# Kernel tuning notes

Hardware: AMD Instinct MI355X
Metric: run time of the kernel (lower is better)

## Reference

```python
import jax, jax.numpy as jnp
import numpy as np
from jax import lax

EPS = 2e-05


def _conv2d(x, w, b, stride):
    # x: [B,C,H,W], w: [O,I,3,3] (OIHW), VALID padding
    y = lax.conv_general_dilated(x, w, (stride, stride), 'VALID',
                                 dimension_numbers=('NCHW', 'OIHW', 'NCHW'))
    return y + b[None, :, None, None]


def _reflect_pad(x):
    return jnp.pad(x, ((0, 0), (0, 0), (1, 1), (1, 1)), mode='reflect')


def _transfer(cont_feat, styl_feat):
    # cont_feat, styl_feat: [B, N, H, W]
    B, N, H, W = cont_feat.shape
    xc = cont_feat.reshape(B, N, -1)   # [B,N,Mc]
    xs = styl_feat.reshape(B, N, -1)   # [B,N,Ms]
    I = jnp.eye(N, dtype=xc.dtype)

    # whitening of content
    mc = jnp.mean(xc, axis=-1, keepdims=True)
    xc0 = xc - mc
    cov_c = jnp.einsum('bnm,bkm->bnk', xc0, xc0) / (xc0.shape[-1] - 1)
    Lc = jnp.linalg.cholesky(cov_c + EPS * I)  # eps*I regularization (torch retry loop)
    inv_Lc = jnp.linalg.inv(Lc)
    whiten = jnp.einsum('bnk,bkm->bnm', inv_Lc, xc0)

    # coloring with style statistics
    ms = jnp.mean(xs, axis=-1, keepdims=True)
    xs0 = xs - ms
    cov_s = jnp.einsum('bnm,bkm->bnk', xs0, xs0) / (xs0.shape[-1] - 1)
    Ls = jnp.linalg.cholesky(cov_s + EPS * I)
    colored = jnp.einsum('bnk,bkm->bnm', Ls, whiten) + ms
    return colored.reshape(B, N, H, W)


def setup_inputs() -> dict:
    key = jax.random.key(0)
    k1, k2, k3, k4 = jax.random.split(key, 4)
    B, C, H, W = 8, 128, 256, 256
    cont_feat = jax.random.normal(k1, (B, C, H, W), dtype=jnp.float32)
    styl_feat = jax.random.normal(k2, (B, C, H, W), dtype=jnp.float32)
    # conv params (kaiming-ish scaling)
    fan1 = C * 9
    W1 = jax.random.normal(k3, (C, C, 3, 3), dtype=jnp.float32) / np.sqrt(fan1)
    b1 = jnp.zeros((C,), dtype=jnp.float32)
    W2 = jax.random.normal(k4, (2 * C, C, 3, 3), dtype=jnp.float32) / np.sqrt(fan1)
    b2 = jnp.zeros((2 * C,), dtype=jnp.float32)
    return {'cont_feat': cont_feat, 'styl_feat': styl_feat,
            'W1': W1, 'b1': b1, 'W2': W2, 'b2': b2}


def reference(cont_feat, styl_feat, W1, b1, W2, b2):
    cs = _transfer(cont_feat, styl_feat)          # [B,C,H,W]
    x = _conv2d(_reflect_pad(cs), W1, b1, 2)      # [B,C,H/2,W/2]
    x = jax.nn.relu(x)
    out = _conv2d(_reflect_pad(x), W2, b2, 1)     # [B,2C,H/2,W/2]
    return out
```

## Files before the change

kernel.cpp:

```cpp
#include <hip/hip_runtime.h>
#include <hip/hip_bf16.h>

#define B_  8
#define C_  128
#define M_  65536
#define EPSV 2e-05f

typedef __attribute__((ext_vector_type(8))) short bf16x8;
typedef __attribute__((ext_vector_type(4))) float f32x4;

#define MFMA(a, b, c) __builtin_amdgcn_mfma_f32_16x16x32_bf16((a), (b), (c), 0, 0, 0)

__device__ __forceinline__ short f2b(float f) {
    unsigned u = __float_as_uint(f);
    u = (u + 0x7FFFu + ((u >> 16) & 1u)) >> 16;
    return (short)u;
}

__device__ __forceinline__ int swz(int px, int c) {
    return px * 256 + ((((c >> 3) ^ (px & 15)) << 4) | ((c & 7) << 1));
}

__device__ __forceinline__ int rot(int i, int k) {
    return i * 128 + ((((k >> 2) + i) & 31) << 2) + (k & 3);
}

__global__ __launch_bounds__(256) void k_prep(const float* W1, const float* W2,
                                              short* wp1, short* wp2) {
    int idx = blockIdx.x * 256 + threadIdx.x;
    if (idx < 9 * 128 * 128) {
        int c = idx & 127, o = (idx >> 7) & 127, rs = idx >> 14;
        wp1[idx] = f2b(W1[(o * 128 + c) * 9 + rs]);
    }
    idx -= 9 * 128 * 128;
    if (idx >= 0 && idx < 9 * 256 * 128) {
        int c = idx & 127, o = (idx >> 7) & 255, rs = idx >> 15;
        wp2[idx] = f2b(W2[(o * 128 + c) * 9 + rs]);
    }
}

__global__ __launch_bounds__(256, 2) void k_gram(const float* cont, const float* styl,
                                                 float* part, float* S) {
    __shared__ short ls[2][128 * 72];
    int bx = blockIdx.x;
    int chunk = bx & 31, which = (bx >> 5) & 1, b = bx >> 6;
    const float* X = (which ? styl : cont) + (size_t)b * C_ * M_ + chunk * 2048;
    int tid = threadIdx.x, lane = tid & 63, wid = tid >> 6;
    int kg = tid & 15, r0 = tid >> 4;

    float sacc[8];
    #pragma unroll
    for (int p = 0; p < 8; ++p) sacc[p] = 0.f;
    f32x4 acc[2][8];
    for (int u = 0; u < 2; ++u)
        for (int j = 0; j < 8; ++j) acc[u][j] = (f32x4){0.f, 0.f, 0.f, 0.f};

    float4 pf[8];
    #pragma unroll
    for (int p = 0; p < 8; ++p)
        pf[p] = *(const float4*)(X + (size_t)(r0 + p * 16) * M_ + kg * 4);

    for (int it = 0; it < 32; ++it) {
        short* lb = ls[it & 1];
        #pragma unroll
        for (int p = 0; p < 8; ++p) {
            int row = r0 + p * 16;
            float4 v = pf[p];
            sacc[p] += v.x + v.y + v.z + v.w;
            union { __hip_bfloat162 h[2]; unsigned long long u; } pk;
            pk.h[0] = __float22bfloat162_rn(make_float2(v.x, v.y));
            pk.h[1] = __float22bfloat162_rn(make_float2(v.z, v.w));
            *(unsigned long long*)(lb + row * 72 + kg * 4) = pk.u;
        }
        if (it < 31) {
            int kb = (it + 1) * 64;
            #pragma unroll
            for (int p = 0; p < 8; ++p)
                pf[p] = *(const float4*)(X + (size_t)(r0 + p * 16) * M_ + kb + kg * 4);
        }
        asm volatile("s_waitcnt lgkmcnt(0)" ::: "memory");
        __builtin_amdgcn_sched_barrier(0);
        __builtin_amdgcn_s_barrier();
        for (int ks = 0; ks < 2; ++ks) {
            int co = ks * 32 + (lane >> 4) * 8;
            bf16x8 a[2], bbf[8];
            for (int u = 0; u < 2; ++u) {
                int row = (wid * 2 + u) * 16 + (lane & 15);
                a[u] = *(const bf16x8*)(lb + row * 72 + co);
            }
            for (int j = 0; j < 8; ++j) {
                int row = j * 16 + (lane & 15);
                bbf[j] = *(const bf16x8*)(lb + row * 72 + co);
            }
            for (int u = 0; u < 2; ++u)
                for (int j = 0; j < 8; ++j)
                    acc[u][j] = MFMA(a[u], bbf[j], acc[u][j]);
        }
    }
    float* Sp = S + ((size_t)which * 8 + b) * 128;
    #pragma unroll
    for (int p = 0; p < 8; ++p) {
        float s = sacc[p];
        s += __shfl_xor(s, 1); s += __shfl_xor(s, 2);
        s += __shfl_xor(s, 4); s += __shfl_xor(s, 8);
        if (kg == 0) atomicAdd(&Sp[r0 + p * 16], s);
    }
    float* Pp = part + ((size_t)((which * 8 + b) * 32 + chunk)) * 16384;
    for (int u = 0; u < 2; ++u) {
        int rowb = (wid * 2 + u) * 16 + (lane >> 4) * 4;
        for (int j = 0; j < 8; ++j) {
            int col = j * 16 + (lane & 15);
            for (int e = 0; e < 4; ++e)
                Pp[(rowb + e) * 128 + col] = acc[u][j][e];
        }
    }
}

__global__ __launch_bounds__(256) void k_gsum(const float* part, float* G) {
    int idx = blockIdx.x * 256 + threadIdx.x;
    int m = idx >> 14, e = idx & 16383;
    const float* p = part + (size_t)m * 32 * 16384 + e;
    float s = 0.f;
    #pragma unroll
    for (int c = 0; c < 32; ++c) s += p[(size_t)c * 16384];
    G[idx] = s;
}

__global__ __launch_bounds__(256) void k_solve(const float* G, const float* S,
                                               short* Tb, float* Vv) {
    __shared__ float A[16384];
    __shared__ float Bm[16384];
    __shared__ float muA[128], muB[128];
    int b = blockIdx.x;
    int tid = threadIdx.x;
    int half = tid >> 7, i = tid & 127;
    const float invM = 1.f / 65536.f;
    const float invM1 = 1.f / 65535.f;
    float* M = half ? Bm : A;
    float* mu = half ? muB : muA;
    const float* Gp = G + ((size_t)(half * 8 + b)) * 16384;
    const float* Sp = S + ((size_t)(half * 8 + b)) * 128;

    mu[i] = Sp[i] * invM;
    __syncthreads();

    {
        const float4* G4 = (const float4*)Gp;
        int c4 = i & 31;
        #pragma unroll 4
        for (int bt = 0; bt < 4; ++bt) {
            float4 gv[8];
            #pragma unroll
            for (int q = 0; q < 8; ++q) gv[q] = G4[i + 128 * (bt * 8 + q)];
            #pragma unroll
            for (int q = 0; q < 8; ++q) {
                int it = bt * 8 + q;
                int r = (i >> 5) + 4 * it;
                float mur = mu[r] * 65536.f;
                float4 mc = *(const float4*)&mu[c4 * 4];
                float4 g = gv[q], cv;
                cv.x = (g.x - mur * mc.x) * invM1;
                cv.y = (g.y - mur * mc.y) * invM1;
                cv.z = (g.z - mur * mc.z) * invM1;
                cv.w = (g.w - mur * mc.w) * invM1;
                int c0 = c4 * 4;
                if (r == c0 + 0) cv.x += EPSV;
                if (r == c0 + 1) cv.y += EPSV;
                if (r == c0 + 2) cv.z += EPSV;
                if (r == c0 + 3) cv.w += EPSV;
                *(float4*)(M + r * 128 + (((c4 + r) & 31) << 2)) = cv;
            }
        }
    }
    __syncthreads();

    #pragma unroll 1
    for (int bb = 0; bb < 4; ++bb) {
        const int jb0 = bb * 32, bend = jb0 + 32;
        float t[32], u[32], t0[32];
        #pragma unroll
        for (int g = 0; g < 8; ++g) {
            float4 v = *(const float4*)(M + i * 128 + ((((jb0 >> 2) + g + i) & 31) << 2));
            t0[g * 4 + 0] = v.x; t0[g * 4 + 1] = v.y;
            t0[g * 4 + 2] = v.z; t0[g * 4 + 3] = v.w;
        }
        #pragma unroll
        for (int jj = 0; jj < 32; ++jj) {
            const int j = jb0 + jj;
            float dot = 0.f;
            #pragma unroll
            for (int kk = 0; kk < jj; ++kk)
                dot += u[kk] * M[rot(j, jb0 + kk)];
            float raw = t0[jj] - dot;
            if (i >= j) M[rot(i, j)] = raw;
            __syncthreads();
            float pr = M[rot(j, j)];
            float piv = sqrtf(pr);
            float rpj = 1.f / piv;
            float tv = (i > j) ? raw * rpj : (i == j ? piv : 0.f);
            t[jj] = tv;
            u[jj] = tv * rpj;
        }
        #pragma unroll
        for (int g = 0; g < 8; ++g) {
            float4 v = {t[g * 4], t[g * 4 + 1], t[g * 4 + 2], t[g * 4 + 3]};
            *(float4*)(M + i * 128 + ((((jb0 >> 2) + g + i) & 31) << 2)) =
                (i >= jb0) ? v : *(float4*)(M + i * 128 + ((((jb0 >> 2) + g + i) & 31) << 2));
        }
        __syncthreads();
        if (bb < 3) {
            if (i >= bend) {
                int jmax = (i & ~63) + 64;
                for (int j4 = bend; j4 < jmax; j4 += 4) {
                    float* rp_ = M + i * 128 + ((((j4 >> 2) + i) & 31) << 2);
                    float4 r = *(float4*)rp_;
                    #pragma unroll
                    for (int g = 0; g < 8; ++g) {
                        int kc = (jb0 >> 2) + g;
                        float4 c0 = *(const float4*)(M + (j4 + 0) * 128 + (((kc + j4 + 0) & 31) << 2));
                        float4 c1 = *(const float4*)(M + (j4 + 1) * 128 + (((kc + j4 + 1) & 31) << 2));
                        float4 c2 = *(const float4*)(M + (j4 + 2) * 128 + (((kc + j4 + 2) & 31) << 2));
                        float4 c3 = *(const float4*)(M + (j4 + 3) * 128 + (((kc + j4 + 3) & 31) << 2));
                        float ta = t[g * 4], tb = t[g * 4 + 1], tc = t[g * 4 + 2], td = t[g * 4 + 3];
                        r.x -= ta * c0.x + tb * c0.y + tc * c0.z + td * c0.w;
                        r.y -= ta * c1.x + tb * c1.y + tc * c1.z + td * c1.w;
                        r.z -= ta * c2.x + tb * c2.y + tc * c2.z + td * c2.w;
                        r.w -= ta * c3.x + tb * c3.y + tc * c3.z + td * c3.w;
                    }
                    *(float4*)rp_ = r;
                }
            }
            __syncthreads();
        }
    }
    __syncthreads();

    float rdia = 0.f, tii = 0.f;
    if (half == 0) {
        rdia = 1.f / A[rot(i, i)];
        tii = Bm[rot(i, i)] * rdia;
    }
    __syncthreads();
    if (half == 0) {
        A[rot(i, i)] = rdia;
        Bm[rot(i, i)] = tii;
    }
    __syncthreads();

    #pragma unroll 1
    for (int b2 = 3; b2 >= 0; --b2) {
        const int jb0 = b2 * 32, bend = jb0 + 32;
        if (half == 0) {
            float t[32], l0[32];
            #pragma unroll
            for (int g = 0; g < 8; ++g) {
                float4 v = *(const float4*)(Bm + i * 128 + ((((jb0 >> 2) + g + i) & 31) << 2));
                l0[g * 4 + 0] = v.x; l0[g * 4 + 1] = v.y;
                l0[g * 4 + 2] = v.z; l0[g * 4 + 3] = v.w;
            }
            #pragma unroll
            for (int jj = 31; jj >= 0; --jj) {
                const int j = jb0 + jj;
                float dot = (i < bend) ? tii * A[rot(i, j)] : 0.f;
                #pragma unroll
                for (int kk = jj + 1; kk < 32; ++kk) {
                    const int k = jb0 + kk;
                    dot += t[kk] * A[rot(k, j)];
                }
                float val = (l0[jj] - dot) * A[rot(j, j)];
                t[jj] = (j < i) ? val : (j == i ? tii : 0.f);
            }
            #pragma unroll
            for (int g = 0; g < 8; ++g) {
                float4 v = {t[g * 4], t[g * 4 + 1], t[g * 4 + 2], t[g * 4 + 3]};
                *(float4*)(Bm + i * 128 + ((((jb0 >> 2) + g + i) & 31) << 2)) = v;
            }
        }
        __syncthreads();
        if (jb0 > 0) {
            if (i >= jb0) {
                float th[32];
                #pragma unroll
                for (int g = 0; g < 8; ++g) {
                    float4 v = *(const float4*)(Bm + i * 128 + ((((jb0 >> 2) + g + i) & 31) << 2));
                    th[g * 4 + 0] = v.x; th[g * 4 + 1] = v.y;
                    th[g * 4 + 2] = v.z; th[g * 4 + 3] = v.w;
                }
                for (int j4 = half * 4; j4 < jb0; j4 += 8) {
                    float* rp = Bm + i * 128 + ((((j4 >> 2) + i) & 31) << 2);
                    float4 r = *(float4*)rp;
                    #pragma unroll
                    for (int kk = 0; kk < 32; ++kk) {
                        const int k = jb0 + kk;
                        float4 lc = *(const float4*)(A + k * 128 + ((((j4 >> 2) + k) & 31) << 2));
                        r.x -= th[kk] * lc.x; r.y -= th[kk] * lc.y;
                        r.z -= th[kk] * lc.z; r.w -= th[kk] * lc.w;
                    }
                    *(float4*)rp = r;
                }
            }
            __syncthreads();
        }
    }

    if (half == 0) {
        float vdot = 0.f;
        short* Tr = Tb + (size_t)b * 16384 + i * 128;
        for (int j4 = 0; j4 < 32; ++j4) {
            float4 tv = *(const float4*)(Bm + i * 128 + (((j4 + i) & 31) << 2));
            float4 mc = *(const float4*)&muA[j4 * 4];
            vdot += tv.x * mc.x + tv.y * mc.y + tv.z * mc.z + tv.w * mc.w;
            union { __hip_bfloat162 h[2]; unsigned long long u; } pk;
            pk.h[0] = __float22bfloat162_rn(make_float2(tv.x, tv.y));
            pk.h[1] = __float22bfloat162_rn(make_float2(tv.z, tv.w));
            *(unsigned long long*)(Tr + j4 * 4) = pk.u;
        }
        Vv[b * 128 + i] = muB[i] - vdot;
    }
}

__global__ __launch_bounds__(256) void k_transform(const float* cont, const short* Tb,
                                                   const float* Vv, short* colored) {
    __shared__ short ls[16384];
    char* lsb = (char*)ls;
    int bx = blockIdx.x;
    int b = bx >> 9, p0 = (bx & 511) << 7;
    int tid = threadIdx.x, lane = tid & 63, wid = tid >> 6;

    {
        int px = tid & 127, ch = tid >> 7;
        const float* Xp = cont + (size_t)b * C_ * M_ + p0 + px;
        for (int it = 0; it < 16; ++it) {
            int c0 = it * 8 + ch * 4;
            float x0 = Xp[(size_t)(c0 + 0) * M_];
            float x1 = Xp[(size_t)(c0 + 1) * M_];
            float x2 = Xp[(size_t)(c0 + 2) * M_];
            float x3 = Xp[(size_t)(c0 + 3) * M_];
            union { short s[4]; unsigned long long u; } pk;
            pk.s[0] = f2b(x0); pk.s[1] = f2b(x1); pk.s[2] = f2b(x2); pk.s[3] = f2b(x3);
            *(unsigned long long*)(lsb + swz(px, c0)) = pk.u;
        }
    }
    __syncthreads();
    f32x4 acc[8][2];
    for (int pg = 0; pg < 8; ++pg)
        for (int u = 0; u < 2; ++u) acc[pg][u] = (f32x4){0.f, 0.f, 0.f, 0.f};
    const short* Tbase = Tb + (size_t)b * 16384;
    for (int kc = 0; kc < 4; ++kc) {
        int co = kc * 32 + (lane >> 4) * 8;
        bf16x8 bfr[2], afr[8];
        for (int u = 0; u < 2; ++u) {
            int chn = (wid * 2 + u) * 16 + (lane & 15);
            bfr[u] = *(const bf16x8*)(Tbase + chn * 128 + co);
        }
        for (int pg = 0; pg < 8; ++pg) {
            int px = pg * 16 + (lane & 15);
            afr[pg] = *(const bf16x8*)(lsb + swz(px, co));
        }
        for (int pg = 0; pg < 8; ++pg)
            for (int u = 0; u < 2; ++u)
                acc[pg][u] = MFMA(afr[pg], bfr[u], acc[pg][u]);
    }
    __syncthreads();
    for (int u = 0; u < 2; ++u) {
        int chn = (wid * 2 + u) * 16 + (lane & 15);
        float vv = Vv[b * 128 + chn];
        for (int pg = 0; pg < 8; ++pg)
            for (int e = 0; e < 4; ++e) {
                int px = pg * 16 + (lane >> 4) * 4 + e;
                *(short*)(lsb + swz(px, chn)) = f2b(acc[pg][u][e] + vv);
            }
    }
    __syncthreads();
    short* dst = colored + ((size_t)b * M_ + p0) * 128;
    for (int it = 0; it < 8; ++it) {
        int gid = tid + it * 256;
        int px = gid >> 4, gr = gid & 15;
        bf16x8 v = *(const bf16x8*)(lsb + px * 256 + ((gr ^ (px & 15)) << 4));
        *(bf16x8*)(dst + (size_t)px * 128 + gr * 8) = v;
    }
}

__global__ __launch_bounds__(256) void k_conv1(const short* colored, const short* wp1,
                                               const float* b1, short* out1) {
    __shared__ short ls[130 * 128];
    char* lsb = (char*)ls;
    int x0 = blockIdx.x * 64, y = blockIdx.y, b = blockIdx.z;
    int tid = threadIdx.x, lane = tid & 63, wid = tid >> 6;

    f32x4 acc[4][2];
    for (int pg = 0; pg < 4; ++pg)
        for (int u = 0; u < 2; ++u) acc[pg][u] = (f32x4){0.f, 0.f, 0.f, 0.f};

    for (int r = 0; r < 3; ++r) {
        int grow = 2 * y - 1 + r;
        if (grow < 0) grow = -grow;
        __syncthreads();
        const short* src = colored + ((size_t)b * M_ + grow * 256) * 128;
        for (int it = 0; it < 9; ++it) {
            int gid = tid + it * 256;
            if (gid < 130 * 16) {
                int L = gid >> 4, gr = gid & 15;
                int gcol = 2 * x0 - 1 + L;
                if (gcol < 0) gcol = -gcol;
                else if (gcol > 255) gcol = 510 - gcol;
                bf16x8 v = *(const bf16x8*)(src + (size_t)gcol * 128 + gr * 8);
                *(bf16x8*)(lsb + L * 256 + ((gr ^ (L & 15)) << 4)) = v;
            }
        }
        __syncthreads();
        for (int s = 0; s < 3; ++s)
            for (int kc = 0; kc < 4; ++kc) {
                int co = kc * 32 + (lane >> 4) * 8;
                bf16x8 afr[4], bfr[2];
                for (int pg = 0; pg < 4; ++pg) {
                    int L = (pg * 16 + (lane & 15)) * 2 + s;
                    afr[pg] = *(const bf16x8*)(lsb + swz(L, co));
                }
                const short* wb = wp1 + (r * 3 + s) * 128 * 128;
                for (int u = 0; u < 2; ++u) {
                    int o = (wid * 2 + u) * 16 + (lane & 15);
                    bfr[u] = *(const bf16x8*)(wb + o * 128 + co);
                }
                for (int pg = 0; pg < 4; ++pg)
                    for (int u = 0; u < 2; ++u)
                        acc[pg][u] = MFMA(afr[pg], bfr[u], acc[pg][u]);
            }
    }
    __syncthreads();
    for (int u = 0; u < 2; ++u) {
        int o = (wid * 2 + u) * 16 + (lane & 15);
        float bias = b1[o];
        for (int pg = 0; pg < 4; ++pg)
            for (int e = 0; e < 4; ++e) {
                int px = pg * 16 + (lane >> 4) * 4 + e;
                float v = acc[pg][u][e] + bias;
                v = v > 0.f ? v : 0.f;
                *(short*)(lsb + swz(px, o)) = f2b(v);
            }
    }
    __syncthreads();
    short* dst = out1 + ((size_t)b * 16384 + y * 128 + x0) * 128;
    for (int it = 0; it < 4; ++it) {
        int gid = tid + it * 256;
        int px = gid >> 4, gr = gid & 15;
        bf16x8 v = *(const bf16x8*)(lsb + px * 256 + ((gr ^ (px & 15)) << 4));
        *(bf16x8*)(dst + (size_t)px * 128 + gr * 8) = v;
    }
}

__global__ __launch_bounds__(256) void k_conv2(const short* out1, const short* wp2,
                                               const float* b2, float* outp) {
    __shared__ short ls[66 * 128];
    char* lsb = (char*)ls;
    int x0 = blockIdx.x * 64, y = blockIdx.y, b = blockIdx.z;
    int tid = threadIdx.x, lane = tid & 63, wid = tid >> 6;

    f32x4 acc[4][4];
    for (int pg = 0; pg < 4; ++pg)
        for (int u = 0; u < 4; ++u) acc[pg][u] = (f32x4){0.f, 0.f, 0.f, 0.f};

    for (int r = 0; r < 3; ++r) {
        int grow = y - 1 + r;
        if (grow < 0) grow = -grow;
        else if (grow > 127) grow = 254 - grow;
        __syncthreads();
        const short* src = out1 + ((size_t)b * 16384 + grow * 128) * 128;
        for (int it = 0; it < 5; ++it) {
            int gid = tid + it * 256;
            if (gid < 66 * 16) {
                int L = gid >> 4, gr = gid & 15;
                int gcol = x0 - 1 + L;
                if (gcol < 0) gcol = -gcol;
                else if (gcol > 127) gcol = 254 - gcol;
                bf16x8 v = *(const bf16x8*)(src + (size_t)gcol * 128 + gr * 8);
                *(bf16x8*)(lsb + L * 256 + ((gr ^ (L & 15)) << 4)) = v;
            }
        }
        __syncthreads();
        for (int s = 0; s < 3; ++s)
            for (int kc = 0; kc < 4; ++kc) {
                int co = kc * 32 + (lane >> 4) * 8;
                bf16x8 afr[4], bfr[4];
                for (int pg = 0; pg < 4; ++pg) {
                    int L = pg * 16 + (lane & 15) + s;
                    afr[pg] = *(const bf16x8*)(lsb + swz(L, co));
                }
                const short* wb = wp2 + (r * 3 + s) * 256 * 128;
                for (int u = 0; u < 4; ++u) {
                    int o = (wid * 4 + u) * 16 + (lane & 15);
                    bfr[u] = *(const bf16x8*)(wb + o * 128 + co);
                }
                for (int pg = 0; pg < 4; ++pg)
                    for (int u = 0; u < 4; ++u)
                        acc[pg][u] = MFMA(afr[pg], bfr[u], acc[pg][u]);
            }
    }
    for (int u = 0; u < 4; ++u) {
        int o = (wid * 4 + u) * 16 + (lane & 15);
        float bias = b2[o];
        float* dst = outp + ((size_t)b * 256 + o) * 16384 + y * 128 + x0;
        for (int pg = 0; pg < 4; ++pg) {
            float4 v;
            v.x = acc[pg][u][0] + bias;
            v.y = acc[pg][u][1] + bias;
            v.z = acc[pg][u][2] + bias;
            v.w = acc[pg][u][3] + bias;
            *(float4*)(dst + pg * 16 + (lane >> 4) * 4) = v;
        }
    }
}

extern "C" void kernel_launch(void* const* d_in, const int* in_sizes, int n_in,
                              void* d_out, int out_size, void* d_ws, size_t ws_size,
                              hipStream_t stream) {
    const float* cont = (const float*)d_in[0];
    const float* styl = (const float*)d_in[1];
    const float* W1 = (const float*)d_in[2];
    const float* b1 = (const float*)d_in[3];
    const float* W2 = (const float*)d_in[4];
    const float* b2 = (const float*)d_in[5];
    float* outp = (float*)d_out;
    char* ws = (char*)d_ws;

    float* G       = (float*)(ws + 0x0);
    float* S       = (float*)(ws + 0x100000);
    short* Tb      = (short*)(ws + 0x110000);
    float* Vv      = (float*)(ws + 0x150000);
    short* wp1     = (short*)(ws + 0x160000);
    short* wp2     = (short*)(ws + 0x1A8000);
    short* colored = (short*)(ws + 0x400000);
    float* part    = (float*)(ws + 0x400000);
    short* out1    = (short*)(ws + 0x8400000);

    hipMemsetAsync(S, 0, 0x2000, stream);
    k_prep<<<1728, 256, 0, stream>>>(W1, W2, wp1, wp2);
    k_gram<<<512, 256, 0, stream>>>(cont, styl, part, S);
    k_gsum<<<1024, 256, 0, stream>>>(part, G);
    k_solve<<<8, 256, 0, stream>>>(G, S, Tb, Vv);
    k_transform<<<4096, 256, 0, stream>>>(cont, Tb, Vv, colored);
    k_conv1<<<dim3(2, 128, 8), 256, 0, stream>>>(colored, wp1, b1, out1);
    k_conv2<<<dim3(2, 128, 8), 256, 0, stream>>>(out1, wp2, b2, outp);
}
```

Before: 656.5 us.

## Stage wider 256-column tiles in gram kernel with full-wave row loads

The gram kernel now stages 256 columns per iteration in a single LDS buffer instead of 64 columns in a double buffer, so each wave loads whole 1KB row segments with all 64 lanes contiguous. Global loads are interleaved with bf16 conversion and LDS stores through two register sets, and each barrier is followed by 8 MFMA k-steps instead of 2. This is meant to coalesce global reads better and halve barrier frequency relative to compute. The cost is losing the overlap of the next tile's global prefetch with MFMA compute, plus more LDS use, which may lower occupancy, and more registers for the row sums.

```diff
diff --git a/kernel.cpp b/kernel.cpp
--- a/kernel.cpp
+++ b/kernel.cpp
@@ -41,69 +41,80 @@
 
 __global__ __launch_bounds__(256, 2) void k_gram(const float* cont, const float* styl,
                                                  float* part, float* S) {
-    __shared__ short ls[2][128 * 72];
+    __shared__ short ls[128 * 264];
     int bx = blockIdx.x;
     int chunk = bx & 31, which = (bx >> 5) & 1, b = bx >> 6;
     const float* X = (which ? styl : cont) + (size_t)b * C_ * M_ + chunk * 2048;
     int tid = threadIdx.x, lane = tid & 63, wid = tid >> 6;
-    int kg = tid & 15, r0 = tid >> 4;
-
-    float sacc[8];
+
+    float sacc[32];
     #pragma unroll
-    for (int p = 0; p < 8; ++p) sacc[p] = 0.f;
+    for (int p = 0; p < 32; ++p) sacc[p] = 0.f;
     f32x4 acc[2][8];
     for (int u = 0; u < 2; ++u)
         for (int j = 0; j < 8; ++j) acc[u][j] = (f32x4){0.f, 0.f, 0.f, 0.f};
 
-    float4 pf[8];
-    #pragma unroll
-    for (int p = 0; p < 8; ++p)
-        pf[p] = *(const float4*)(X + (size_t)(r0 + p * 16) * M_ + kg * 4);
-
-    for (int it = 0; it < 32; ++it) {
-        short* lb = ls[it & 1];
-        #pragma unroll
-        for (int p = 0; p < 8; ++p) {
-            int row = r0 + p * 16;
-            float4 v = pf[p];
-            sacc[p] += v.x + v.y + v.z + v.w;
-            union { __hip_bfloat162 h[2]; unsigned long long u; } pk;
-            pk.h[0] = __float22bfloat162_rn(make_float2(v.x, v.y));
-            pk.h[1] = __float22bfloat162_rn(make_float2(v.z, v.w));
-            *(unsigned long long*)(lb + row * 72 + kg * 4) = pk.u;
-        }
-        if (it < 31) {
-            int kb = (it + 1) * 64;
-            #pragma unroll
-            for (int p = 0; p < 8; ++p)
-                pf[p] = *(const float4*)(X + (size_t)(r0 + p * 16) * M_ + kb + kg * 4);
-        }
+    float4 pfA[8], pfB[8];
+
+#define GLOAD(pf, g)                                                              \
+    _Pragma("unroll")                                                             \
+    for (int p = 0; p < 8; ++p)                                                   \
+        pf[p] = *(const float4*)(X + (size_t)(wid + 4 * ((g) * 8 + p)) * M_ +     \
+                                 kb + lane * 4);
+
+#define GSTORE(pf, g)                                                             \
+    _Pragma("unroll")                                                             \
+    for (int p = 0; p < 8; ++p) {                                                 \
+        int row = wid + 4 * ((g) * 8 + p);                                        \
+        float4 v = pf[p];                                                         \
+        sacc[(g) * 8 + p] += v.x + v.y + v.z + v.w;                               \
+        union { __hip_bfloat162 h[2]; unsigned long long u; } pk;                 \
+        pk.h[0] = __float22bfloat162_rn(make_float2(v.x, v.y));                   \
+        pk.h[1] = __float22bfloat162_rn(make_float2(v.z, v.w));                   \
+        *(unsigned long long*)(ls + row * 264 + lane * 4) = pk.u;                 \
+    }
+
+    for (int it = 0; it < 8; ++it) {
+        int kb = it * 256;
+        GLOAD(pfA, 0)
+        GLOAD(pfB, 1)
+        GSTORE(pfA, 0)
+        GLOAD(pfA, 2)
+        GSTORE(pfB, 1)
+        GLOAD(pfB, 3)
+        GSTORE(pfA, 2)
+        GSTORE(pfB, 3)
         asm volatile("s_waitcnt lgkmcnt(0)" ::: "memory");
         __builtin_amdgcn_sched_barrier(0);
         __builtin_amdgcn_s_barrier();
-        for (int ks = 0; ks < 2; ++ks) {
+        for (int ks = 0; ks < 8; ++ks) {
             int co = ks * 32 + (lane >> 4) * 8;
             bf16x8 a[2], bbf[8];
             for (int u = 0; u < 2; ++u) {
                 int row = (wid * 2 + u) * 16 + (lane & 15);
-                a[u] = *(const bf16x8*)(lb + row * 72 + co);
+                a[u] = *(const bf16x8*)(ls + row * 264 + co);
             }
             for (int j = 0; j < 8; ++j) {
                 int row = j * 16 + (lane & 15);
-                bbf[j] = *(const bf16x8*)(lb + row * 72 + co);
+                bbf[j] = *(const bf16x8*)(ls + row * 264 + co);
             }
             for (int u = 0; u < 2; ++u)
                 for (int j = 0; j < 8; ++j)
                     acc[u][j] = MFMA(a[u], bbf[j], acc[u][j]);
         }
-    }
+        __builtin_amdgcn_sched_barrier(0);
+        __builtin_amdgcn_s_barrier();
+    }
+#undef GLOAD
+#undef GSTORE
     float* Sp = S + ((size_t)which * 8 + b) * 128;
     #pragma unroll
-    for (int p = 0; p < 8; ++p) {
+    for (int p = 0; p < 32; ++p) {
         float s = sacc[p];
         s += __shfl_xor(s, 1); s += __shfl_xor(s, 2);
         s += __shfl_xor(s, 4); s += __shfl_xor(s, 8);
-        if (kg == 0) atomicAdd(&Sp[r0 + p * 16], s);
+        s += __shfl_xor(s, 16); s += __shfl_xor(s, 32);
+        if (lane == 0) atomicAdd(&Sp[wid + 4 * p], s);
     }
     float* Pp = part + ((size_t)((which * 8 + b) * 32 + chunk)) * 16384;
     for (int u = 0; u < 2; ++u) {
```

Result: no change. 652.3 us (-0.6%).
